# Kernel tuning notes

Hardware: AMD Instinct MI355X
Metric: run time of the kernel (lower is better)

The kernel has to match this reference:

```python
import jax, jax.numpy as jnp
import numpy as np

N, E, G = 50000, 400000, 64
DIN, HID, H, ED = 128, 32, 8, 5
HC = H * HID            # 256, conv3 out_channels (concat=False, heads=1)
LH, DOUT = 256, 32
NEG_SLOPE = 0.2


def setup_inputs() -> dict:
    key = jax.random.key(0)
    ks = jax.random.split(key, 32)
    rn = lambda k, s, sc=0.05: (jax.random.normal(k, s, jnp.float32) * sc)
    inp = {
        "x": jax.random.normal(ks[0], (N, DIN), jnp.float32),
        "edge_index": jax.random.randint(ks[1], (2, E), 0, N, jnp.int32),
        "edge_attr": jax.random.uniform(ks[2], (E, ED), jnp.float32),
        "batch": jnp.sort(jax.random.randint(ks[3], (N,), 0, G, jnp.int32)),
        # conv1: in=DIN, heads=H, out=HID, concat=True
        "W1": rn(ks[4], (DIN, H * HID)), "as1": rn(ks[5], (H, HID)), "ad1": rn(ks[6], (H, HID)),
        "We1": rn(ks[7], (ED, H * HID)), "ae1": rn(ks[8], (H, HID)), "b1": jnp.zeros((H * HID,), jnp.float32),
        # conv2: in=H*HID, heads=H, out=HID, concat=True
        "W2": rn(ks[9], (H * HID, H * HID)), "as2": rn(ks[10], (H, HID)), "ad2": rn(ks[11], (H, HID)),
        "We2": rn(ks[12], (ED, H * HID)), "ae2": rn(ks[13], (H, HID)), "b2": jnp.zeros((H * HID,), jnp.float32),
        # conv3: in=H*HID, heads=1, out=HC, concat=False
        "W3": rn(ks[14], (H * HID, HC)), "as3": rn(ks[15], (1, HC)), "ad3": rn(ks[16], (1, HC)),
        "We3": rn(ks[17], (ED, HC)), "ae3": rn(ks[18], (1, HC)), "b3": jnp.zeros((HC,), jnp.float32),
        # MLP head
        "fcW1": rn(ks[19], (HC, LH)), "fcb1": jnp.zeros((LH,), jnp.float32),
        "fcW2": rn(ks[20], (LH, DOUT)), "fcb2": jnp.zeros((DOUT,), jnp.float32),
    }
    return inp


def gat_layer(x, src, dst, ea, W, att_s, att_d, We, att_e, bias, heads, out_ch, concat):
    n = x.shape[0]
    h = (x @ W).reshape(n, heads, out_ch)                 # [N,H,C]
    e = (ea @ We).reshape(-1, heads, out_ch)              # [E,H,C]
    a_s = (h * att_s).sum(-1)                             # [N,H]
    a_d = (h * att_d).sum(-1)                             # [N,H]
    a_e = (e * att_e).sum(-1)                             # [E,H]
    alpha = jax.nn.leaky_relu(a_s[src] + a_d[dst] + a_e, NEG_SLOPE)  # [E,H]
    m = jax.ops.segment_max(alpha, dst, num_segments=n)   # segment softmax over dst
    p = jnp.exp(alpha - m[dst])
    denom = jax.ops.segment_sum(p, dst, num_segments=n)
    w = p / (denom[dst] + 1e-16)                          # [E,H]
    msg = h[src] * w[:, :, None]                          # [E,H,C]
    out = jax.ops.segment_sum(msg, dst, num_segments=n)   # [N,H,C]
    out = out.reshape(n, heads * out_ch) if concat else out.mean(axis=1)
    return out + bias


def reference(x, edge_index, edge_attr, batch,
              W1, as1, ad1, We1, ae1, b1,
              W2, as2, ad2, We2, ae2, b2,
              W3, as3, ad3, We3, ae3, b3,
              fcW1, fcb1, fcW2, fcb2):
    src, dst = edge_index[0], edge_index[1]
    h = jax.nn.elu(gat_layer(x, src, dst, edge_attr, W1, as1, ad1, We1, ae1, b1, H, HID, True))
    h = jax.nn.elu(gat_layer(h, src, dst, edge_attr, W2, as2, ad2, We2, ae2, b2, H, HID, True))
    h = jax.nn.elu(gat_layer(h, src, dst, edge_attr, W3, as3, ad3, We3, ae3, b3, 1, HC, False))
    h = jax.nn.gelu(h @ fcW1 + fcb1, approximate=False) @ fcW2 + fcb2   # [N,DOUT]
    # global_mean_pool over batch ids
    sums = jax.ops.segment_sum(h, batch, num_segments=G)
    cnt = jax.ops.segment_sum(jnp.ones((h.shape[0],), h.dtype), batch, num_segments=G)
    return sums / jnp.maximum(cnt, 1.0)[:, None]
```

## Files before the change

### kernel.cpp

```cpp
#include <hip/hip_runtime.h>
#include <math.h>


#define N_NODES 50000
#define N_EDGES 400000
#define N_GRAPH 64
#define DIN     128
#define NHC     256
#define DOUT    32

typedef _Float16 f16x8 __attribute__((ext_vector_type(8)));
typedef _Float16 f16x4 __attribute__((ext_vector_type(4)));
typedef float    f32x4 __attribute__((ext_vector_type(4)));

#define LDP2 72

__device__ __forceinline__ void fma_mix_lo(float& acc, float pj, int w) {
    asm volatile("v_fma_mix_f32 %0, %1, %2, %0 op_sel:[0,0,0] op_sel_hi:[0,1,0]"
                 : "+v"(acc) : "v"(pj), "v"(w));
}
__device__ __forceinline__ void fma_mix_hi(float& acc, float pj, int w) {
    asm volatile("v_fma_mix_f32 %0, %1, %2, %0 op_sel:[0,1,0] op_sel_hi:[0,1,0]"
                 : "+v"(acc) : "v"(pj), "v"(w));
}

__global__ __launch_bounds__(256) void mfma_gemm_kernel(
    const _Float16* __restrict__ Ah, const _Float16* __restrict__ Bh,
    const float* __restrict__ bias, _Float16* __restrict__ Ch,
    const float* __restrict__ asl, const float* __restrict__ adl,
    float* __restrict__ asb, float* __restrict__ adb,
    const int* __restrict__ batch, float* __restrict__ pooled,
    int nrow, int K, int mode)
{
    __shared__ __align__(16) _Float16 sAh[128][LDP2];
    __shared__ __align__(16) _Float16 sBh[64][LDP2];

    const int tid = threadIdx.x, lane = tid & 63, wid = tid >> 6;
    const int wm = wid & 1, wn = wid >> 1;

    int xt, yt;
    if (gridDim.x == 4) {
        int bid = blockIdx.x + (blockIdx.y << 2);
        yt = (bid >> 5) * 8 + (bid & 7);
        xt = (bid >> 3) & 3;
    } else { xt = blockIdx.x; yt = blockIdx.y; }
    const int row0 = yt * 128, col0 = xt * 64;
    if (row0 >= nrow) return;

    const int frow = lane & 15, fk = (lane >> 4) * 8;

    f32x4 acc[4][2] = {};
    f16x8 pA[4], pB[2];

#pragma unroll
    for (int p = 0; p < 4; p++) {
        int idx = tid + p * 256;
        int r = idx >> 3, ch = (idx & 7) * 8;
        int gr = row0 + r;
        pA[p] = (gr < nrow) ? *(const f16x8*)(Ah + (long)gr * K + ch) : (f16x8)0;
    }
#pragma unroll
    for (int p = 0; p < 2; p++) {
        int idx = tid + p * 256;
        int r = idx >> 3, ch = (idx & 7) * 8;
        pB[p] = *(const f16x8*)(Bh + (long)(col0 + r) * K + ch);
    }

    for (int k0 = 0; k0 < K; k0 += 64) {
#pragma unroll
        for (int p = 0; p < 4; p++) {
            int idx = tid + p * 256;
            *(f16x8*)&sAh[idx >> 3][(idx & 7) * 8] = pA[p];
        }
#pragma unroll
        for (int p = 0; p < 2; p++) {
            int idx = tid + p * 256;
            *(f16x8*)&sBh[idx >> 3][(idx & 7) * 8] = pB[p];
        }
        __syncthreads();

        if (k0 + 64 < K) {
            int kn = k0 + 64;
#pragma unroll
            for (int p = 0; p < 4; p++) {
                int idx = tid + p * 256;
                int r = idx >> 3, ch = (idx & 7) * 8;
                int gr = row0 + r;
                pA[p] = (gr < nrow) ? *(const f16x8*)(Ah + (long)gr * K + kn + ch) : (f16x8)0;
            }
#pragma unroll
            for (int p = 0; p < 2; p++) {
                int idx = tid + p * 256;
                int r = idx >> 3, ch = (idx & 7) * 8;
                pB[p] = *(const f16x8*)(Bh + (long)(col0 + r) * K + kn + ch);
            }
        }

#pragma unroll
        for (int sub = 0; sub < 2; sub++) {
            const int fks = fk + sub * 32;
            f16x8 bh[2];
#pragma unroll
            for (int nt = 0; nt < 2; nt++)
                bh[nt] = *(const f16x8*)&sBh[wn * 32 + nt * 16 + frow][fks];
#pragma unroll
            for (int mt = 0; mt < 4; mt++) {
                f16x8 ah = *(const f16x8*)&sAh[wm * 64 + mt * 16 + frow][fks];
#pragma unroll
                for (int nt = 0; nt < 2; nt++)
                    acc[mt][nt] = __builtin_amdgcn_mfma_f32_16x16x32_f16(ah, bh[nt], acc[mt][nt], 0, 0, 0);
            }
        }
        __syncthreads();
    }

    const int crow0 = row0 + wm * 64 + (lane >> 4) * 4;
    const int ccol0 = col0 + wn * 32 + (lane & 15);

    if (mode == 0) {
#pragma unroll
        for (int mt = 0; mt < 4; mt++)
#pragma unroll
            for (int nt = 0; nt < 2; nt++) {
                int col = ccol0 + nt * 16;
#pragma unroll
                for (int r = 0; r < 4; r++) {
                    int row = crow0 + mt * 16 + r;
                    if (row < nrow) Ch[(long)row * 256 + col] = (_Float16)acc[mt][nt][r];
                }
            }
        if (asl != nullptr) {
            const float asl0 = asl[ccol0], asl1 = asl[ccol0 + 16];
            const float adl0 = adl[ccol0], adl1 = adl[ccol0 + 16];
            const int headw = (col0 + wn * 32) >> 5;
#pragma unroll
            for (int mt = 0; mt < 4; mt++) {
#pragma unroll
                for (int r = 0; r < 4; r++) {
                    float s = acc[mt][0][r] * asl0 + acc[mt][1][r] * asl1;
                    float d = acc[mt][0][r] * adl0 + acc[mt][1][r] * adl1;
                    s += __shfl_xor(s, 1); s += __shfl_xor(s, 2);
                    s += __shfl_xor(s, 4); s += __shfl_xor(s, 8);
                    d += __shfl_xor(d, 1); d += __shfl_xor(d, 2);
                    d += __shfl_xor(d, 4); d += __shfl_xor(d, 8);
                    if ((lane & 15) == 0) {
                        int row = crow0 + mt * 16 + r;
                        if (row < nrow) {
                            asb[row * 8 + headw] = s;
                            adb[row * 8 + headw] = d;
                        }
                    }
                }
            }
        }
    } else {
        float* pool = (float*)&sAh[0][0];
        const int g0 = batch[row0];
        const int rlast = (row0 + 127 < nrow) ? row0 + 127 : nrow - 1;
        const int gspan = batch[rlast] - g0 + 1;
        const bool fits = (gspan <= 16);
        for (int i = tid; i < 16 * 64; i += 256) pool[i] = 0.f;
        __syncthreads();

        const float b0 = bias[ccol0], b1 = bias[ccol0 + 16];
        const int lc0 = ccol0 - col0, lc1 = lc0 + 16;
        float sum0 = 0.f, sum1 = 0.f;
        int curg = -1;
#pragma unroll
        for (int mt = 0; mt < 4; mt++) {
#pragma unroll
            for (int r = 0; r < 4; r++) {
                int row = crow0 + mt * 16 + r;
                if (row >= nrow) continue;
                int g = batch[row];
                if (g != curg) {
                    if (curg >= 0) {
                        if (fits) {
                            atomicAdd(&pool[(curg - g0) * 64 + lc0], sum0);
                            atomicAdd(&pool[(curg - g0) * 64 + lc1], sum1);
                        } else {
                            atomicAdd(&pooled[curg * 256 + ccol0], sum0);
                            atomicAdd(&pooled[curg * 256 + ccol0 + 16], sum1);
                        }
                    }
                    curg = g; sum0 = 0.f; sum1 = 0.f;
                }
                float v0 = acc[mt][0][r] + b0;
                float v1 = acc[mt][1][r] + b1;
                sum0 += 0.5f * v0 * (1.f + erff(v0 * 0.7071067811865475f));
                sum1 += 0.5f * v1 * (1.f + erff(v1 * 0.7071067811865475f));
            }
        }
        if (curg >= 0) {
            if (fits) {
                atomicAdd(&pool[(curg - g0) * 64 + lc0], sum0);
                atomicAdd(&pool[(curg - g0) * 64 + lc1], sum1);
            } else {
                atomicAdd(&pooled[curg * 256 + ccol0], sum0);
                atomicAdd(&pooled[curg * 256 + ccol0 + 16], sum1);
            }
        }
        __syncthreads();
        if (fits) {
            for (int i = tid; i < gspan * 64; i += 256) {
                float val = pool[i];
                if (val != 0.f)
                    atomicAdd(&pooled[(g0 + (i >> 6)) * 256 + col0 + (i & 63)], val);
            }
        }
    }
}

#define J0 1600000
#define J1 32768
#define J2 65536
#define J3 65536
#define J4 65536
#define J5 16384
#define J6 N_NODES
#define J7 64
#define JTOT (J0+J1+J2+J3+J4+J5+J6+J7)

__device__ __forceinline__ void t_one(const float* W, _Float16* Bh,
                                      int id, int K, int realN)
{
    int n = id / K, k = id - n * K;
    Bh[id] = (_Float16)W[(long)k * realN + n];
}

__global__ __launch_bounds__(256) void prep_kernel(
    const float* __restrict__ x,
    const float* __restrict__ W1, const float* __restrict__ W2, const float* __restrict__ W3,
    const float* __restrict__ F1,
    _Float16* __restrict__ xh,
    _Float16* __restrict__ W1th, _Float16* __restrict__ W2th,
    _Float16* __restrict__ W3th, _Float16* __restrict__ F1th,
    float* __restrict__ pooled, int* __restrict__ deg, int* __restrict__ gcnt)
{
    int idx = blockIdx.x * 256 + threadIdx.x;
    if (idx < J0) {
        float4 v = ((const float4*)x)[idx];
        f16x4 h;
        h[0] = (_Float16)v.x; h[1] = (_Float16)v.y;
        h[2] = (_Float16)v.z; h[3] = (_Float16)v.w;
        *(f16x4*)(xh + (long)idx * 4) = h;
        return;
    }
    idx -= J0;
    if (idx < J1) { t_one(W1, W1th, idx, DIN, NHC); return; }
    idx -= J1;
    if (idx < J2) { t_one(W2, W2th, idx, NHC, NHC); return; }
    idx -= J2;
    if (idx < J3) { t_one(W3, W3th, idx, NHC, NHC); return; }
    idx -= J3;
    if (idx < J4) { t_one(F1, F1th, idx, NHC, NHC); return; }
    idx -= J4;
    if (idx < J5) { pooled[idx] = 0.f; return; }
    idx -= J5;
    if (idx < J6) { deg[idx] = 0; return; }
    idx -= J6;
    if (idx < J7) { gcnt[idx] = 0; return; }
}

__global__ void me_all_kernel(
    const float* __restrict__ We1, const float* __restrict__ ae1,
    const float* __restrict__ We2, const float* __restrict__ ae2,
    const float* __restrict__ We3, const float* __restrict__ ae3,
    float* __restrict__ MeAll)
{
    int l = blockIdx.x;
    const float* We = (l == 0) ? We1 : (l == 1) ? We2 : We3;
    const float* ae = (l == 0) ? ae1 : (l == 1) ? ae2 : ae3;
    int H = (l == 2) ? 1 : 8, C = (l == 2) ? 256 : 32;
    int t = threadIdx.x;
    if (t >= 5 * H) return;
    int j = t / H, hh = t - j * H;
    float s = 0.f;
    for (int c = 0; c < C; c++) s += We[j * NHC + hh * C + c] * ae[hh * C + c];
    MeAll[l * 40 + j * H + hh] = s;
}

__global__ __launch_bounds__(256) void count_hist_kernel(
    const int* __restrict__ ei, const int* __restrict__ batch,
    int* __restrict__ deg, int* __restrict__ gcnt, int E, int N)
{
    __shared__ int hist[N_GRAPH];
    int t = threadIdx.x;
    if (t < N_GRAPH) hist[t] = 0;
    __syncthreads();
    int i = blockIdx.x * 256 + t;
    if (i < E) atomicAdd(&deg[ei[E + i]], 1);
    if (i < N) atomicAdd(&hist[batch[i]], 1);
    __syncthreads();
    if (t < N_GRAPH && hist[t] > 0) atomicAdd(&gcnt[t], hist[t]);
}

__global__ __launch_bounds__(256) void scan_block_kernel(
    const int* __restrict__ deg, int* __restrict__ rowstart, int* __restrict__ partial, int n)
{
    __shared__ int s[256];
    int i = blockIdx.x * 256 + threadIdx.x;
    int v = (i < n) ? deg[i] : 0;
    s[threadIdx.x] = v;
    __syncthreads();
    for (int off = 1; off < 256; off <<= 1) {
        int t = (threadIdx.x >= off) ? s[threadIdx.x - off] : 0;
        __syncthreads();
        s[threadIdx.x] += t;
        __syncthreads();
    }
    if (i < n) rowstart[i] = s[threadIdx.x] - v;
    if (threadIdx.x == 255) partial[blockIdx.x] = s[255];
}

__global__ __launch_bounds__(256) void scan_partial_kernel(int* __restrict__ partial, int nb)
{
    __shared__ int s[256];
    int v = (threadIdx.x < nb) ? partial[threadIdx.x] : 0;
    s[threadIdx.x] = v;
    __syncthreads();
    for (int off = 1; off < 256; off <<= 1) {
        int t = (threadIdx.x >= off) ? s[threadIdx.x - off] : 0;
        __syncthreads();
        s[threadIdx.x] += t;
        __syncthreads();
    }
    if (threadIdx.x < nb) partial[threadIdx.x] = s[threadIdx.x] - v;
}

__global__ __launch_bounds__(256) void scan_add_kernel(
    int* __restrict__ rowstart, const int* __restrict__ partial, int* __restrict__ cursor,
    int n, int E)
{
    int i = blockIdx.x * 256 + threadIdx.x;
    if (i < n) {
        int v = rowstart[i] + partial[blockIdx.x];
        rowstart[i] = v;
        cursor[i] = v;
    }
    if (i == 0) rowstart[n] = E;
}

__global__ __launch_bounds__(256) void fill_kernel(
    const int* __restrict__ ei, int* __restrict__ cursor, int2* __restrict__ csr2, int E)
{
    int e = blockIdx.x * 256 + threadIdx.x;
    if (e >= E) return;
    int dst = ei[E + e];
    int pos = atomicAdd(&cursor[dst], 1);
    csr2[pos] = make_int2(ei[e], e);
}

__global__ __launch_bounds__(256) void aec_kernel(
    const int2* __restrict__ csr2, const float* __restrict__ ea,
    const float* __restrict__ MeAll,
    int* __restrict__ csr, _Float16* __restrict__ aec, int E)
{
    int pos = blockIdx.x * 256 + threadIdx.x;
    if (pos >= E) return;
    int2 se = csr2[pos];
    csr[pos] = se.x;
    const float* eap = ea + (long)se.y * 5;
    float e0 = eap[0], e1 = eap[1], e2 = eap[2], e3 = eap[3], e4 = eap[4];
#pragma unroll
    for (int l = 0; l < 2; l++) {
        const float* Me = MeAll + l * 40;
        f16x8 v;
#pragma unroll
        for (int hh = 0; hh < 8; hh++) {
            float s = e0 * Me[hh] + e1 * Me[8 + hh] + e2 * Me[16 + hh]
                    + e3 * Me[24 + hh] + e4 * Me[32 + hh];
            v[hh] = (_Float16)s;
        }
        *(f16x8*)(aec + (long)l * N_EDGES * 8 + (long)pos * 8) = v;
    }
    const float* Me2 = MeAll + 80;
    float s2 = e0 * Me2[0] + e1 * Me2[1] + e2 * Me2[2] + e3 * Me2[3] + e4 * Me2[4];
    f16x8 v2;
#pragma unroll
    for (int hh = 0; hh < 8; hh++) v2[hh] = (_Float16)s2;
    *(f16x8*)(aec + (long)2 * N_EDGES * 8 + (long)pos * 8) = v2;
}

__global__ __launch_bounds__(256) void gat_agg_kernel(
    const int* __restrict__ rowstart, const int* __restrict__ csr,
    const _Float16* __restrict__ aec, const float* __restrict__ asb,
    const float* __restrict__ adb,
    const _Float16* __restrict__ h, const float* __restrict__ bias,
    _Float16* __restrict__ Oh, int H, int clog2)
{
    int node = blockIdx.x * 4 + (threadIdx.x >> 6);
    if (node >= N_NODES) return;
    const int lane = threadIdx.x & 63;
    const int half = lane >> 5;
    const int c8   = (lane & 31) * 8;
    const int hc   = c8 >> clog2;
    const int heff = lane & (H - 1);
    const int grp  = lane >> 3;

    float adn;
    if (H == 1) {
        float t = adb[node * 8 + (lane & 7)];
        t += __shfl_xor(t, 1); t += __shfl_xor(t, 2); t += __shfl_xor(t, 4);
        adn = t;
    } else {
        adn = adb[node * 8 + heff];
    }
    const int beg = rowstart[node], end = rowstart[node + 1];

    float acc[8] = {};
    float den = 0.f;

    for (int i = beg; i < end; i += 8) {
        int idx = i + grp;
        const bool valid = (idx < end);
        if (!valid) idx = end - 1;
        const int sj = csr[idx];
        const float ae = (float)aec[(long)idx * 8 + heff];
        float asv;
        if (H == 1) {
            float t = asb[sj * 8 + (lane & 7)];
            t += __shfl_xor(t, 1); t += __shfl_xor(t, 2); t += __shfl_xor(t, 4);
            asv = t;
        } else {
            asv = asb[sj * 8 + heff];
        }
        float al = asv + adn + ae;
        al = fmaxf(al, 0.2f * al);
        const float pv = valid ? __expf(al) : 0.f;
#pragma unroll
        for (int jj = 0; jj < 4; jj++) {
            const int j = jj * 2 + half;
            const float pj = __shfl(pv, j * 8 + hc);
            const int srcj = __shfl(sj, j * 8);
            const int4 hw = *(const int4*)(h + (long)srcj * NHC + c8);
            den += pj;
            fma_mix_lo(acc[0], pj, hw.x); fma_mix_hi(acc[1], pj, hw.x);
            fma_mix_lo(acc[2], pj, hw.y); fma_mix_hi(acc[3], pj, hw.y);
            fma_mix_lo(acc[4], pj, hw.z); fma_mix_hi(acc[5], pj, hw.z);
            fma_mix_lo(acc[6], pj, hw.w); fma_mix_hi(acc[7], pj, hw.w);
        }
    }

    den += __shfl_xor(den, 32);
#pragma unroll
    for (int k = 0; k < 8; k++)
        acc[k] += __shfl_xor(acc[k], 32);

    if (half == 0) {
        const float w = 1.0f / (den + 1e-16f);
        const float4 b0 = *(const float4*)(bias + c8);
        const float4 b1 = *(const float4*)(bias + c8 + 4);
        const float bb[8] = {b0.x, b0.y, b0.z, b0.w, b1.x, b1.y, b1.z, b1.w};
        f16x8 oh;
#pragma unroll
        for (int k = 0; k < 8; k++) {
            float v = acc[k] * w + bb[k];
            v = (v > 0.f) ? v : (__expf(v) - 1.f);
            oh[k] = (_Float16)v;
        }
        *(f16x8*)(Oh + (long)node * NHC + c8) = oh;
    }
}

__global__ void final_kernel(const float* __restrict__ pooled, const int* __restrict__ gcnt,
                             const float* __restrict__ fcW2, const float* __restrict__ fcb2,
                             float* __restrict__ out)
{
    int g = blockIdx.x;
    int j = threadIdx.x;
    if (j >= DOUT) return;
    float s = 0.f;
    for (int k = 0; k < NHC; k++) s += pooled[g * NHC + k] * fcW2[k * DOUT + j];
    int c = gcnt[g];
    out[g * DOUT + j] = (c > 0) ? (s / (float)c + fcb2[j]) : 0.f;
}

extern "C" void kernel_launch(void* const* d_in, const int* in_sizes, int n_in,
                              void* d_out, int out_size, void* d_ws, size_t ws_size,
                              hipStream_t stream)
{
    const float* x    = (const float*)d_in[0];
    const int*   ei   = (const int*)  d_in[1];
    const float* ea   = (const float*)d_in[2];
    const int*   bat  = (const int*)  d_in[3];
    const float* W[3]   = {(const float*)d_in[4],  (const float*)d_in[10], (const float*)d_in[16]};
    const float* Asl[3] = {(const float*)d_in[5],  (const float*)d_in[11], (const float*)d_in[17]};
    const float* Adl[3] = {(const float*)d_in[6],  (const float*)d_in[12], (const float*)d_in[18]};
    const float* Wel[3] = {(const float*)d_in[7],  (const float*)d_in[13], (const float*)d_in[19]};
    const float* Ael[3] = {(const float*)d_in[8],  (const float*)d_in[14], (const float*)d_in[20]};
    const float* Bil[3] = {(const float*)d_in[9],  (const float*)d_in[15], (const float*)d_in[21]};
    const float* fcW1 = (const float*)d_in[22];
    const float* fcb1 = (const float*)d_in[23];
    const float* fcW2 = (const float*)d_in[24];
    const float* fcb2 = (const float*)d_in[25];

    char* w = (char*)d_ws;
    _Float16* h    = (_Float16*)w;     w += (size_t)N_NODES * NHC * 2;
    _Float16* xh   = (_Float16*)w;     w += (size_t)N_NODES * DIN * 2;
    _Float16* xbh  = (_Float16*)w;     w += (size_t)N_NODES * NHC * 2;
    float*    asb  = (float*)w;        w += (size_t)N_NODES * 8 * 4;
    float*    adb  = (float*)w;        w += (size_t)N_NODES * 8 * 4;
    float*    MeAll= (float*)w;        w += 120 * 4;
    float*    pooled=(float*)w;        w += (size_t)N_GRAPH * NHC * 4;
    _Float16* W1th = (_Float16*)w;     w += (size_t)NHC * DIN * 2;
    _Float16* W2th = (_Float16*)w;     w += (size_t)NHC * NHC * 2;
    _Float16* W3th = (_Float16*)w;     w += (size_t)NHC * NHC * 2;
    _Float16* F1th = (_Float16*)w;     w += (size_t)NHC * NHC * 2;
    int* gcnt     = (int*)w;           w += N_GRAPH * 4;
    int* deg      = (int*)w;           w += (size_t)N_NODES * 4;
    int* rowstart = (int*)w;           w += (size_t)(N_NODES + 1) * 4;
    int* cursor   = (int*)w;           w += (size_t)N_NODES * 4;
    int* partial  = (int*)w;           w += 256 * 4;
    w = (char*)(((size_t)w + 15) & ~(size_t)15);
    int2* csr2    = (int2*)w;          w += (size_t)N_EDGES * 8;
    int* csr      = (int*)w;           w += (size_t)N_EDGES * 4;
    w = (char*)(((size_t)w + 15) & ~(size_t)15);
    _Float16* aec = (_Float16*)w;      w += (size_t)3 * N_EDGES * 8 * 2;

    const int NB = (N_NODES + 255) / 256;

    prep_kernel<<<(JTOT + 255) / 256, 256, 0, stream>>>(
        x, W[0], W[1], W[2], fcW1,
        xh, W1th, W2th, W3th, F1th,
        pooled, deg, gcnt);
    count_hist_kernel<<<(N_EDGES + 255) / 256, 256, 0, stream>>>(ei, bat, deg, gcnt, N_EDGES, N_NODES);
    scan_block_kernel<<<NB, 256, 0, stream>>>(deg, rowstart, partial, N_NODES);
    scan_partial_kernel<<<1, 256, 0, stream>>>(partial, NB);
    scan_add_kernel<<<NB, 256, 0, stream>>>(rowstart, partial, cursor, N_NODES, N_EDGES);
    me_all_kernel<<<3, 64, 0, stream>>>(Wel[0], Ael[0], Wel[1], Ael[1], Wel[2], Ael[2], MeAll);
    fill_kernel<<<(N_EDGES + 255) / 256, 256, 0, stream>>>(ei, cursor, csr2, N_EDGES);
    aec_kernel<<<(N_EDGES + 255) / 256, 256, 0, stream>>>(csr2, ea, MeAll, csr, aec, N_EDGES);

    const int Hs[3] = {8, 8, 1};
    const int CL[3] = {5, 5, 8};
    const int Ks[3] = {DIN, NHC, NHC};

    const dim3 ggrid(4, 392);

    const _Float16* curh = xh;
    const _Float16* Wth[3] = {W1th, W2th, W3th};
    for (int l = 0; l < 3; l++) {
        const int H = Hs[l];
        mfma_gemm_kernel<<<ggrid, 256, 0, stream>>>(
            curh, Wth[l], nullptr, h,
            Asl[l], Adl[l], asb, adb,
            nullptr, nullptr,
            N_NODES, Ks[l], 0);
        gat_agg_kernel<<<(N_NODES + 3) / 4, 256, 0, stream>>>(
            rowstart, csr, aec + (size_t)l * N_EDGES * 8, asb, adb, h, Bil[l], xbh, H, CL[l]);
        curh = xbh;
    }

    mfma_gemm_kernel<<<ggrid, 256, 0, stream>>>(
        xbh, F1th, fcb1, nullptr,
        nullptr, nullptr, nullptr, nullptr,
        bat, pooled,
        N_NODES, NHC, 3);
    final_kernel<<<N_GRAPH, 64, 0, stream>>>(pooled, gcnt, fcW2, fcb2, (float*)d_out);
}
```

Baseline: 435.8 us.

## Fold setup kernels into prep, merge scan stages, atomically reduce layer-3 attention scores

Moves the edge-attention coefficient computation and the zeroing of new layer-3 score buffers into the prep kernel, and merges the partial-scan and scan-add kernels into one kernel in which every block rescans the block totals. For the single-head layer, the GEMM epilogue now atomically adds per-column-tile partial scores into a single slot, so the aggregation kernel no longer needs the shuffle reduction over 8 partials. This cuts two kernel launches and some aggregation work, at the cost of extra float atomics in the GEMM epilogue and a redundant small scan per block.

```diff
diff --git a/kernel.cpp b/kernel.cpp
--- a/kernel.cpp
+++ b/kernel.cpp
@@ -30,7 +30,7 @@
     const float* __restrict__ asl, const float* __restrict__ adl,
     float* __restrict__ asb, float* __restrict__ adb,
     const int* __restrict__ batch, float* __restrict__ pooled,
-    int nrow, int K, int mode)
+    int nrow, int K, int accum, int mode)
 {
     __shared__ __align__(16) _Float16 sAh[128][LDP2];
     __shared__ __align__(16) _Float16 sBh[64][LDP2];
@@ -146,8 +146,13 @@
                     if ((lane & 15) == 0) {
                         int row = crow0 + mt * 16 + r;
                         if (row < nrow) {
-                            asb[row * 8 + headw] = s;
-                            adb[row * 8 + headw] = d;
+                            if (accum) {
+                                atomicAdd(&asb[row * 8], s);
+                                atomicAdd(&adb[row * 8], d);
+                            } else {
+                                asb[row * 8 + headw] = s;
+                                adb[row * 8 + headw] = d;
+                            }
                         }
                     }
                 }
@@ -219,7 +224,9 @@
 #define J5 16384
 #define J6 N_NODES
 #define J7 64
-#define JTOT (J0+J1+J2+J3+J4+J5+J6+J7)
+#define J8 N_NODES
+#define J9 85
+#define JTOT (J0+J1+J2+J3+J4+J5+J6+J7+J8+J9)
 
 __device__ __forceinline__ void t_one(const float* W, _Float16* Bh,
                                       int id, int K, int realN)
@@ -232,10 +239,14 @@
     const float* __restrict__ x,
     const float* __restrict__ W1, const float* __restrict__ W2, const float* __restrict__ W3,
     const float* __restrict__ F1,
+    const float* __restrict__ We1, const float* __restrict__ ae1,
+    const float* __restrict__ We2, const float* __restrict__ ae2,
+    const float* __restrict__ We3, const float* __restrict__ ae3,
     _Float16* __restrict__ xh,
     _Float16* __restrict__ W1th, _Float16* __restrict__ W2th,
     _Float16* __restrict__ W3th, _Float16* __restrict__ F1th,
-    float* __restrict__ pooled, int* __restrict__ deg, int* __restrict__ gcnt)
+    float* __restrict__ pooled, int* __restrict__ deg, int* __restrict__ gcnt,
+    float* __restrict__ asb3, float* __restrict__ adb3, float* __restrict__ MeAll)
 {
     int idx = blockIdx.x * 256 + threadIdx.x;
     if (idx < J0) {
@@ -260,24 +271,21 @@
     if (idx < J6) { deg[idx] = 0; return; }
     idx -= J6;
     if (idx < J7) { gcnt[idx] = 0; return; }
-}
-
-__global__ void me_all_kernel(
-    const float* __restrict__ We1, const float* __restrict__ ae1,
-    const float* __restrict__ We2, const float* __restrict__ ae2,
-    const float* __restrict__ We3, const float* __restrict__ ae3,
-    float* __restrict__ MeAll)
-{
-    int l = blockIdx.x;
-    const float* We = (l == 0) ? We1 : (l == 1) ? We2 : We3;
-    const float* ae = (l == 0) ? ae1 : (l == 1) ? ae2 : ae3;
-    int H = (l == 2) ? 1 : 8, C = (l == 2) ? 256 : 32;
-    int t = threadIdx.x;
-    if (t >= 5 * H) return;
-    int j = t / H, hh = t - j * H;
-    float s = 0.f;
-    for (int c = 0; c < C; c++) s += We[j * NHC + hh * C + c] * ae[hh * C + c];
-    MeAll[l * 40 + j * H + hh] = s;
+    idx -= J7;
+    if (idx < J8) { asb3[idx * 8] = 0.f; adb3[idx * 8] = 0.f; return; }
+    idx -= J8;
+    if (idx < J9) {
+        int l, j, hh, H, C;
+        if (idx < 40)      { l = 0; H = 8; C = 32;  j = idx >> 3; hh = idx & 7; }
+        else if (idx < 80) { l = 1; H = 8; C = 32;  int r = idx - 40; j = r >> 3; hh = r & 7; }
+        else               { l = 2; H = 1; C = 256; j = idx - 80; hh = 0; }
+        const float* We = (l == 0) ? We1 : (l == 1) ? We2 : We3;
+        const float* ae = (l == 0) ? ae1 : (l == 1) ? ae2 : ae3;
+        float s = 0.f;
+        for (int c = 0; c < C; c++) s += We[j * NHC + hh * C + c] * ae[hh * C + c];
+        MeAll[l * 40 + j * H + hh] = s;
+        return;
+    }
 }
 
 __global__ __launch_bounds__(256) void count_hist_kernel(
@@ -313,28 +321,24 @@
     if (threadIdx.x == 255) partial[blockIdx.x] = s[255];
 }
 
-__global__ __launch_bounds__(256) void scan_partial_kernel(int* __restrict__ partial, int nb)
-{
-    __shared__ int s[256];
-    int v = (threadIdx.x < nb) ? partial[threadIdx.x] : 0;
-    s[threadIdx.x] = v;
+__global__ __launch_bounds__(256) void scan_add2_kernel(
+    int* __restrict__ rowstart, const int* __restrict__ partial, int* __restrict__ cursor,
+    int n, int E, int nb)
+{
+    __shared__ int sp[256];
+    int t = threadIdx.x;
+    sp[t] = (t < nb) ? partial[t] : 0;
     __syncthreads();
     for (int off = 1; off < 256; off <<= 1) {
-        int t = (threadIdx.x >= off) ? s[threadIdx.x - off] : 0;
-        __syncthreads();
-        s[threadIdx.x] += t;
-        __syncthreads();
-    }
-    if (threadIdx.x < nb) partial[threadIdx.x] = s[threadIdx.x] - v;
-}
-
-__global__ __launch_bounds__(256) void scan_add_kernel(
-    int* __restrict__ rowstart, const int* __restrict__ partial, int* __restrict__ cursor,
-    int n, int E)
-{
-    int i = blockIdx.x * 256 + threadIdx.x;
+        int v = (t >= off) ? sp[t - off] : 0;
+        __syncthreads();
+        sp[t] += v;
+        __syncthreads();
+    }
+    int add = (blockIdx.x == 0) ? 0 : sp[blockIdx.x - 1];
+    int i = blockIdx.x * 256 + t;
     if (i < n) {
-        int v = rowstart[i] + partial[blockIdx.x];
+        int v = rowstart[i] + add;
         rowstart[i] = v;
         cursor[i] = v;
     }
@@ -398,14 +402,7 @@
     const int heff = lane & (H - 1);
     const int grp  = lane >> 3;
 
-    float adn;
-    if (H == 1) {
-        float t = adb[node * 8 + (lane & 7)];
-        t += __shfl_xor(t, 1); t += __shfl_xor(t, 2); t += __shfl_xor(t, 4);
-        adn = t;
-    } else {
-        adn = adb[node * 8 + heff];
-    }
+    const float adn = adb[node * 8 + heff];
     const int beg = rowstart[node], end = rowstart[node + 1];
 
     float acc[8] = {};
@@ -417,15 +414,7 @@
         if (!valid) idx = end - 1;
         const int sj = csr[idx];
         const float ae = (float)aec[(long)idx * 8 + heff];
-        float asv;
-        if (H == 1) {
-            float t = asb[sj * 8 + (lane & 7)];
-            t += __shfl_xor(t, 1); t += __shfl_xor(t, 2); t += __shfl_xor(t, 4);
-            asv = t;
-        } else {
-            asv = asb[sj * 8 + heff];
-        }
-        float al = asv + adn + ae;
+        float al = asb[sj * 8 + heff] + adn + ae;
         al = fmaxf(al, 0.2f * al);
         const float pv = valid ? __expf(al) : 0.f;
 #pragma unroll
@@ -501,6 +490,8 @@
     _Float16* xbh  = (_Float16*)w;     w += (size_t)N_NODES * NHC * 2;
     float*    asb  = (float*)w;        w += (size_t)N_NODES * 8 * 4;
     float*    adb  = (float*)w;        w += (size_t)N_NODES * 8 * 4;
+    float*    asb3 = (float*)w;        w += (size_t)N_NODES * 8 * 4;
+    float*    adb3 = (float*)w;        w += (size_t)N_NODES * 8 * 4;
     float*    MeAll= (float*)w;        w += 120 * 4;
     float*    pooled=(float*)w;        w += (size_t)N_GRAPH * NHC * 4;
     _Float16* W1th = (_Float16*)w;     w += (size_t)NHC * DIN * 2;
@@ -522,13 +513,12 @@
 
     prep_kernel<<<(JTOT + 255) / 256, 256, 0, stream>>>(
         x, W[0], W[1], W[2], fcW1,
+        Wel[0], Ael[0], Wel[1], Ael[1], Wel[2], Ael[2],
         xh, W1th, W2th, W3th, F1th,
-        pooled, deg, gcnt);
+        pooled, deg, gcnt, asb3, adb3, MeAll);
     count_hist_kernel<<<(N_EDGES + 255) / 256, 256, 0, stream>>>(ei, bat, deg, gcnt, N_EDGES, N_NODES);
     scan_block_kernel<<<NB, 256, 0, stream>>>(deg, rowstart, partial, N_NODES);
-    scan_partial_kernel<<<1, 256, 0, stream>>>(partial, NB);
-    scan_add_kernel<<<NB, 256, 0, stream>>>(rowstart, partial, cursor, N_NODES, N_EDGES);
-    me_all_kernel<<<3, 64, 0, stream>>>(Wel[0], Ael[0], Wel[1], Ael[1], Wel[2], Ael[2], MeAll);
+    scan_add2_kernel<<<NB, 256, 0, stream>>>(rowstart, partial, cursor, N_NODES, N_EDGES, NB);
     fill_kernel<<<(N_EDGES + 255) / 256, 256, 0, stream>>>(ei, cursor, csr2, N_EDGES);
     aec_kernel<<<(N_EDGES + 255) / 256, 256, 0, stream>>>(csr2, ea, MeAll, csr, aec, N_EDGES);
 
@@ -542,13 +532,15 @@
     const _Float16* Wth[3] = {W1th, W2th, W3th};
     for (int l = 0; l < 3; l++) {
         const int H = Hs[l];
+        const bool h1 = (l == 2);
         mfma_gemm_kernel<<<ggrid, 256, 0, stream>>>(
             curh, Wth[l], nullptr, h,
-            Asl[l], Adl[l], asb, adb,
+            Asl[l], Adl[l], h1 ? asb3 : asb, h1 ? adb3 : adb,
             nullptr, nullptr,
-            N_NODES, Ks[l], 0);
+            N_NODES, Ks[l], h1 ? 1 : 0, 0);
         gat_agg_kernel<<<(N_NODES + 3) / 4, 256, 0, stream>>>(
-            rowstart, csr, aec + (size_t)l * N_EDGES * 8, asb, adb, h, Bil[l], xbh, H, CL[l]);
+            rowstart, csr, aec + (size_t)l * N_EDGES * 8,
+            h1 ? asb3 : asb, h1 ? adb3 : adb, h, Bil[l], xbh, H, CL[l]);
         curh = xbh;
     }
 
@@ -556,6 +548,6 @@
         xbh, F1th, fcb1, nullptr,
         nullptr, nullptr, nullptr, nullptr,
         bat, pooled,
-        N_NODES, NHC, 3);
+        N_NODES, NHC, 0, 3);
     final_kernel<<<N_GRAPH, 64, 0, stream>>>(pooled, gcnt, fcW2, fcb2, (float*)d_out);
 }
```

After: 456.0 us. +4.6%, slower.
